# Performance work log

Measured on AMD Instinct MI355X. Metric: run time of the kernel, lower is better.

Reference implementation:

```python
import jax, jax.numpy as jnp
import numpy as np
import math

E = 2048        # embed_dim
H = 16          # num_heads
HD = E // H // 2  # head_dim = 64
DEPTH = 12
LAMBDA_INIT = 0.8 - 0.6 * math.exp(-0.3 * DEPTH)


def setup_inputs() -> dict:
    key = jax.random.key(0)
    ks = jax.random.split(key, 9)
    s = 0.02
    return {
        "x": jax.random.normal(ks[0], (2, 2048, E), jnp.float32),
        "Wq": jax.random.normal(ks[1], (E, E), jnp.float32) * s,
        "Wk": jax.random.normal(ks[2], (E, E), jnp.float32) * s,  # n_rep = 1
        "Wv": jax.random.normal(ks[3], (E, E), jnp.float32) * s,
        "Wo": jax.random.normal(ks[4], (E, E), jnp.float32) * s,
        "lq1": jax.random.normal(ks[5], (HD,), jnp.float32) * 0.1,
        "lk1": jax.random.normal(ks[6], (HD,), jnp.float32) * 0.1,
        "lq2": jax.random.normal(ks[7], (HD,), jnp.float32) * 0.1,
        "lk2": jax.random.normal(ks[8], (HD,), jnp.float32) * 0.1,
    }


def reference(x, Wq, Wk, Wv, Wo, lq1, lk1, lq2, lk2):
    b, t, e = x.shape
    scaling = HD ** (-0.5)
    # projections; split into 2*H sub-heads of dim HD for q/k, H heads of 2*HD for v
    q = (x @ Wq).reshape(b, t, 2 * H, HD).transpose(0, 2, 1, 3) * scaling  # [b,2H,t,hd]
    k = (x @ Wk).reshape(b, t, 2 * H, HD).transpose(0, 2, 1, 3)           # [b,2H,t,hd]
    v = (x @ Wv).reshape(b, t, H, 2 * HD).transpose(0, 2, 1, 3)           # [b,H,t,2hd]

    scores = jnp.einsum('bhqd,bhkd->bhqk', q, k)  # [b,2H,t,t]
    causal = jnp.triu(jnp.full((t, t), -jnp.inf, dtype=jnp.float32), 1)
    aw = jax.nn.softmax((scores + causal).astype(jnp.float32), axis=-1)

    lam = (jnp.exp(jnp.sum(lq1 * lk1)) - jnp.exp(jnp.sum(lq2 * lk2)) + LAMBDA_INIT)
    aw = aw.reshape(b, H, 2, t, t)
    aw = aw[:, :, 0] - lam * aw[:, :, 1]  # differential attention

    attn = jnp.einsum('bhqk,bhkd->bhqd', aw, v)  # [b,H,t,2hd]
    # RMSNorm over last dim (no affine), eps=1e-5
    attn = attn * jax.lax.rsqrt(jnp.mean(attn * attn, axis=-1, keepdims=True) + 1e-5)
    attn = attn * (1.0 - LAMBDA_INIT)
    attn = attn.transpose(0, 2, 1, 3).reshape(b, t, H * 2 * HD)
    return attn @ Wo
```

## Files before the change

kernel.cpp:

```cpp
#include <hip/hip_runtime.h>
#include <stdint.h>

typedef __bf16 bf16_t;
typedef __bf16 bf16x8 __attribute__((ext_vector_type(8)));
typedef __bf16 bf16x4 __attribute__((ext_vector_type(4)));
typedef float  f32x4  __attribute__((ext_vector_type(4)));

#define L2E 1.44269504088896340736f
#define LAMBDA_INIT 0.7836057665316245f
#define ONE_MINUS_LAMBDA_INIT 0.2163942334683755f

__device__ __forceinline__ void gload_lds16(const void* g, void* l) {
  __builtin_amdgcn_global_load_lds(
      (const __attribute__((address_space(1))) char*)(uintptr_t)g,
      (__attribute__((address_space(3))) char*)(uintptr_t)l, 16, 0, 0);
}

__device__ __forceinline__ f32x4 mfma_bf16(bf16x8 a, bf16x8 b, f32x4 c) {
  return __builtin_amdgcn_mfma_f32_16x16x32_bf16(a, b, c, 0, 0, 0);
}

__global__ __launch_bounds__(256) void cvt_bf16(const float* __restrict__ in,
                                                bf16_t* __restrict__ out) {
  const size_t idx = ((size_t)blockIdx.x * 256 + threadIdx.x) * 8;
  float4 a = *(const float4*)(in + idx);
  float4 c = *(const float4*)(in + idx + 4);
  bf16x8 v;
  v[0] = (bf16_t)a.x; v[1] = (bf16_t)a.y; v[2] = (bf16_t)a.z; v[3] = (bf16_t)a.w;
  v[4] = (bf16_t)c.x; v[5] = (bf16_t)c.y; v[6] = (bf16_t)c.z; v[7] = (bf16_t)c.w;
  *(bf16x8*)(out + idx) = v;
}

__global__ __launch_bounds__(256) void cvt_wT(const float* __restrict__ W,
                                              bf16_t* __restrict__ WT, float scale) {
  __shared__ float t[64][65];
  const int k0 = blockIdx.x * 64, n0 = blockIdx.y * 64;
  const int r = threadIdx.x >> 2, cg = threadIdx.x & 3;
#pragma unroll
  for (int q = 0; q < 4; ++q) {
    float4 v = *(const float4*)(W + (size_t)(k0 + r) * 2048 + n0 + cg * 16 + q * 4);
    t[r][cg * 16 + q * 4 + 0] = v.x;
    t[r][cg * 16 + q * 4 + 1] = v.y;
    t[r][cg * 16 + q * 4 + 2] = v.z;
    t[r][cg * 16 + q * 4 + 3] = v.w;
  }
  __syncthreads();
  bf16x8 o0, o1;
#pragma unroll
  for (int j = 0; j < 8; ++j) o0[j] = (bf16_t)(t[cg * 16 + j][r] * scale);
#pragma unroll
  for (int j = 0; j < 8; ++j) o1[j] = (bf16_t)(t[cg * 16 + 8 + j][r] * scale);
  bf16_t* dst = WT + (size_t)(n0 + r) * 2048 + k0 + cg * 16;
  *(bf16x8*)dst = o0;
  *(bf16x8*)(dst + 8) = o1;
}

__global__ void lam_kernel(const float* lq1, const float* lk1,
                           const float* lq2, const float* lk2, float* out) {
  const int l = threadIdx.x;
  float p1 = lq1[l] * lk1[l];
  float p2 = lq2[l] * lk2[l];
#pragma unroll
  for (int d = 1; d < 64; d <<= 1) {
    p1 += __shfl_xor(p1, d);
    p2 += __shfl_xor(p2, d);
  }
  if (l == 0) *out = expf(p1) - expf(p2) + LAMBDA_INIT;
}

template <int OUTMODE>
__global__ __launch_bounds__(256, 2) void gemm_bt(const bf16_t* __restrict__ A,
                                                  const bf16_t* __restrict__ Bt,
                                                  void* __restrict__ Cv) {
  __shared__ __align__(16) bf16_t As[128 * 64];
  __shared__ __align__(16) bf16_t Bs[128 * 64];
  const int tid = threadIdx.x;
  const int w = tid >> 6, lane = tid & 63;
  const int wr = w >> 1, wc = w & 1;
  const int lm = lane >> 4, ln = lane & 15;
  const int flat = (int)blockIdx.y * (int)gridDim.x + (int)blockIdx.x;
  const int swz = (flat & 7) * 64 + (flat >> 3);
  const int m0 = (swz & 31) * 128, n0 = (swz >> 5) * 128;

  const f32x4 vzero = {0.f, 0.f, 0.f, 0.f};
  f32x4 acc[4][4];
#pragma unroll
  for (int m = 0; m < 4; ++m)
#pragma unroll
    for (int n = 0; n < 4; ++n) acc[m][n] = vzero;

  for (int k0 = 0; k0 < 2048; k0 += 64) {
    __syncthreads();
#pragma unroll
    for (int j = 0; j < 4; ++j) {
      const int inst = w * 4 + j;
      const int row = inst * 8 + (lane >> 3);
      const int cb = ((lane & 7) * 16) ^ ((row & 7) << 4);
      gload_lds16(A + (size_t)(m0 + row) * 2048 + k0 + (cb >> 1),
                  (char*)As + inst * 1024);
      gload_lds16(Bt + (size_t)(n0 + row) * 2048 + k0 + (cb >> 1),
                  (char*)Bs + inst * 1024);
    }
    asm volatile("s_waitcnt vmcnt(0)" ::: "memory");
    __syncthreads();

#pragma unroll
    for (int kc = 0; kc < 2; ++kc) {
      bf16x8 af[4], bfr[4];
#pragma unroll
      for (int m = 0; m < 4; ++m) {
        const int row = wr * 64 + m * 16 + ln;
        int off = row * 128 + kc * 64 + lm * 16;
        off ^= (row & 7) << 4;
        af[m] = *(const bf16x8*)((const char*)As + off);
      }
#pragma unroll
      for (int n = 0; n < 4; ++n) {
        const int row = wc * 64 + n * 16 + ln;
        int off = row * 128 + kc * 64 + lm * 16;
        off ^= (row & 7) << 4;
        bfr[n] = *(const bf16x8*)((const char*)Bs + off);
      }
      __builtin_amdgcn_s_setprio(1);
#pragma unroll
      for (int m = 0; m < 4; ++m)
#pragma unroll
        for (int n = 0; n < 4; ++n) acc[m][n] = mfma_bf16(af[m], bfr[n], acc[m][n]);
      __builtin_amdgcn_s_setprio(0);
    }
  }

  if (OUTMODE == 0) {
    bf16_t* C = (bf16_t*)Cv;
#pragma unroll
    for (int m = 0; m < 4; ++m)
#pragma unroll
      for (int n = 0; n < 4; ++n)
#pragma unroll
        for (int r = 0; r < 4; ++r) {
          const size_t grow = m0 + wr * 64 + m * 16 + lm * 4 + r;
          const int gcol = n0 + wc * 64 + n * 16 + ln;
          C[grow * 2048 + gcol] = (bf16_t)acc[m][n][r];
        }
  } else if (OUTMODE == 1) {
    bf16_t* C = (bf16_t*)Cv;
#pragma unroll
    for (int m = 0; m < 4; ++m)
#pragma unroll
      for (int n = 0; n < 4; ++n) {
        const size_t gcol = n0 + wc * 64 + n * 16 + ln;
        const int growb = m0 + wr * 64 + m * 16 + lm * 4;
        bf16x4 v;
#pragma unroll
        for (int r = 0; r < 4; ++r) v[r] = (bf16_t)acc[m][n][r];
        *(bf16x4*)(C + gcol * 4096 + growb) = v;
      }
  } else {
    float* C = (float*)Cv;
#pragma unroll
    for (int m = 0; m < 4; ++m)
#pragma unroll
      for (int n = 0; n < 4; ++n)
#pragma unroll
        for (int r = 0; r < 4; ++r) {
          const size_t grow = m0 + wr * 64 + m * 16 + lm * 4 + r;
          const int gcol = n0 + wc * 64 + n * 16 + ln;
          C[grow * 2048 + gcol] = acc[m][n][r];
        }
  }
}

__global__ __launch_bounds__(256, 2) void flash_diff(const bf16_t* __restrict__ Q,
                                                     const bf16_t* __restrict__ K,
                                                     const bf16_t* __restrict__ Vt,
                                                     bf16_t* __restrict__ attnb,
                                                     const float* __restrict__ lamP) {
  __shared__ __align__(16) char smem[81920];
  bf16_t* Ps = (bf16_t*)smem;

  const int tid = threadIdx.x;
  const int w = tid >> 6, lane = tid & 63;
  const int lm = lane >> 4, ln = lane & 15;
  const int h = blockIdx.y, b = blockIdx.z;
  const size_t bt0 = (size_t)b * 2048;
  const float lam = *lamP;

  auto stage_kv = [&](int buf, int k0) {
#pragma unroll
    for (int j = 0; j < 4; ++j) {
      const int inst = w * 4 + j;
      {
        const int row = inst * 4 + (lane >> 4);
        const int cb = ((lane & 15) * 16) ^ ((row & 7) << 4);
        gload_lds16(K + (bt0 + k0 + row) * 2048 + h * 128 + (cb >> 1),
                    smem + 16384 + buf * 16384 + inst * 1024);
      }
      {
        const int row = inst * 8 + (lane >> 3);
        const int cb = ((lane & 7) * 16) ^ ((row & 7) << 4);
        gload_lds16(Vt + (size_t)(h * 128 + row) * 4096 + bt0 + k0 + (cb >> 1),
                    smem + 49152 + buf * 16384 + inst * 1024);
      }
    }
  };

  for (int half = 0; half < 2; ++half) {
    const int qt = half == 0 ? (int)blockIdx.x : 31 - (int)blockIdx.x;
    const int q0 = qt * 64;

#pragma unroll
    for (int j = 0; j < 4; ++j) {
      const int inst = w * 4 + j;
      const int row = inst * 4 + (lane >> 4);
      const int cb = ((lane & 15) * 16) ^ ((row & 7) << 4);
      gload_lds16(Q + (bt0 + q0 + row) * 2048 + h * 128 + (cb >> 1),
                  smem + inst * 1024);
    }
    stage_kv(0, 0);
    asm volatile("s_waitcnt vmcnt(0)" ::: "memory");
    __syncthreads();

    bf16x8 qf[2][2];
#pragma unroll
    for (int s = 0; s < 2; ++s)
#pragma unroll
      for (int kc = 0; kc < 2; ++kc) {
        const int row = w * 16 + ln;
        int off = row * 256 + s * 128 + kc * 64 + lm * 16;
        off ^= (row & 7) << 4;
        qf[s][kc] = *(const bf16x8*)((const char*)smem + off);
      }
    __syncthreads();

    const f32x4 vzero = {0.f, 0.f, 0.f, 0.f};
    f32x4 acc[2][8];
    float lsum[2][4];
#pragma unroll
    for (int s = 0; s < 2; ++s) {
#pragma unroll
      for (int n = 0; n < 8; ++n) acc[s][n] = vzero;
#pragma unroll
      for (int r = 0; r < 4; ++r) lsum[s][r] = 0.f;
    }

    int cur = 0;
    for (int kt = 0; kt <= qt; ++kt) {
      if (kt < qt) stage_kv(cur ^ 1, (kt + 1) * 64);

      const char* Ksb = (const char*)smem + 16384 + cur * 16384;
      const char* Vsb = (const char*)smem + 49152 + cur * 16384;

#pragma unroll
      for (int s = 0; s < 2; ++s) {
        f32x4 sa[4];
#pragma unroll
        for (int n = 0; n < 4; ++n) sa[n] = vzero;
        __builtin_amdgcn_s_setprio(1);
#pragma unroll
        for (int kc = 0; kc < 2; ++kc) {
#pragma unroll
          for (int n = 0; n < 4; ++n) {
            const int row = n * 16 + ln;
            int off = row * 256 + s * 128 + kc * 64 + lm * 16;
            off ^= (row & 7) << 4;
            bf16x8 kf = *(const bf16x8*)(Ksb + off);
            sa[n] = mfma_bf16(qf[s][kc], kf, sa[n]);
          }
        }
        __builtin_amdgcn_s_setprio(0);
        if (kt == qt) {
#pragma unroll
          for (int n = 0; n < 4; ++n)
#pragma unroll
            for (int r = 0; r < 4; ++r) {
              const int kg = n * 16 + ln;
              const int qg = w * 16 + lm * 4 + r;
              if (kg > qg) sa[n][r] = -1e30f;
            }
        }
        bf16_t* pbase = Ps + (w * 2 + s) * 1024;
#pragma unroll
        for (int r = 0; r < 4; ++r) {
          float ps = 0.f;
#pragma unroll
          for (int n = 0; n < 4; ++n) {
            const float p = exp2f(sa[n][r]);
            sa[n][r] = p;
            ps += p;
          }
          lsum[s][r] += ps;
        }
#pragma unroll
        for (int n = 0; n < 4; ++n)
#pragma unroll
          for (int r = 0; r < 4; ++r) {
            const int row = lm * 4 + r;
            int off = row * 128 + (n * 16 + ln) * 2;
            off ^= (row & 7) << 4;
            *(bf16_t*)((char*)pbase + off) = (bf16_t)sa[n][r];
          }
      }

#pragma unroll
      for (int kc = 0; kc < 2; ++kc) {
        bf16x8 pf[2];
#pragma unroll
        for (int s = 0; s < 2; ++s) {
          int off = ln * 128 + kc * 64 + lm * 16;
          off ^= (ln & 7) << 4;
          pf[s] = *(const bf16x8*)((const char*)(Ps + (w * 2 + s) * 1024) + off);
        }
        __builtin_amdgcn_s_setprio(1);
#pragma unroll
        for (int n = 0; n < 8; ++n) {
          const int row = n * 16 + ln;
          int off = row * 128 + kc * 64 + lm * 16;
          off ^= (row & 7) << 4;
          bf16x8 vf = *(const bf16x8*)(Vsb + off);
          acc[0][n] = mfma_bf16(pf[0], vf, acc[0][n]);
          acc[1][n] = mfma_bf16(pf[1], vf, acc[1][n]);
        }
        __builtin_amdgcn_s_setprio(0);
      }

      asm volatile("s_waitcnt vmcnt(0)" ::: "memory");
      __syncthreads();
      cur ^= 1;
    }

#pragma unroll
    for (int r = 0; r < 4; ++r) {
      float l0 = lsum[0][r], l1 = lsum[1][r];
#pragma unroll
      for (int d = 1; d < 16; d <<= 1) {
        l0 += __shfl_xor(l0, d);
        l1 += __shfl_xor(l1, d);
      }
      const float rl0 = 1.0f / l0;
      const float rl1 = 1.0f / l1;
      float o[8];
      float ss = 0.f;
#pragma unroll
      for (int n = 0; n < 8; ++n) {
        const float v = acc[0][n][r] * rl0 - lam * (acc[1][n][r] * rl1);
        o[n] = v;
        ss += v * v;
      }
      ss += __shfl_xor(ss, 1);
      ss += __shfl_xor(ss, 2);
      ss += __shfl_xor(ss, 4);
      ss += __shfl_xor(ss, 8);
      const float sc = rsqrtf(ss * (1.0f / 128.f) + 1e-5f) * ONE_MINUS_LAMBDA_INIT;
      const size_t grow = bt0 + q0 + w * 16 + lm * 4 + r;
#pragma unroll
      for (int n = 0; n < 8; ++n)
        attnb[grow * 2048 + h * 128 + n * 16 + ln] = (bf16_t)(o[n] * sc);
    }
  }
}

extern "C" void kernel_launch(void* const* d_in, const int* in_sizes, int n_in,
                              void* d_out, int out_size, void* d_ws, size_t ws_size,
                              hipStream_t stream) {
  const float* x   = (const float*)d_in[0];
  const float* Wq  = (const float*)d_in[1];
  const float* Wk  = (const float*)d_in[2];
  const float* Wv  = (const float*)d_in[3];
  const float* Wo  = (const float*)d_in[4];
  const float* lq1 = (const float*)d_in[5];
  const float* lk1 = (const float*)d_in[6];
  const float* lq2 = (const float*)d_in[7];
  const float* lk2 = (const float*)d_in[8];

  char* ws = (char*)d_ws;
  bf16_t* xb    = (bf16_t*)(ws + 0);
  bf16_t* wqT   = (bf16_t*)(ws + 16777216);
  bf16_t* wkT   = (bf16_t*)(ws + 25165824);
  bf16_t* wvT   = (bf16_t*)(ws + 33554432);
  bf16_t* woT   = (bf16_t*)(ws + 41943040);
  bf16_t* Qb    = (bf16_t*)(ws + 50331648);
  bf16_t* Kb    = (bf16_t*)(ws + 67108864);
  bf16_t* Vtb   = (bf16_t*)(ws + 16777216);
  bf16_t* attnb = (bf16_t*)(ws + 0);
  float*  lamP  = (float*)(ws + 83886080);

  cvt_bf16<<<4096, 256, 0, stream>>>(x, xb);
  cvt_wT<<<dim3(32, 32), 256, 0, stream>>>(Wq, wqT, 0.125f * L2E);
  cvt_wT<<<dim3(32, 32), 256, 0, stream>>>(Wk, wkT, 1.0f);
  cvt_wT<<<dim3(32, 32), 256, 0, stream>>>(Wv, wvT, 1.0f);
  cvt_wT<<<dim3(32, 32), 256, 0, stream>>>(Wo, woT, 1.0f);
  lam_kernel<<<1, 64, 0, stream>>>(lq1, lk1, lq2, lk2, lamP);

  gemm_bt<0><<<dim3(32, 16), 256, 0, stream>>>(xb, wqT, (void*)Qb);
  gemm_bt<0><<<dim3(32, 16), 256, 0, stream>>>(xb, wkT, (void*)Kb);
  gemm_bt<1><<<dim3(32, 16), 256, 0, stream>>>(xb, wvT, (void*)Vtb);

  flash_diff<<<dim3(16, 16, 2), 256, 0, stream>>>(Qb, Kb, Vtb, attnb, lamP);

  gemm_bt<2><<<dim3(32, 16), 256, 0, stream>>>(attnb, woT, d_out);
}
```

Before: 287.9 us.

## Rewrite flash_diff with 32x32 MFMA, register-resident P via permlane swap

Restructures the differential flash attention kernel so each wave handles 32 queries for one sub-head using 32x32x16 MFMA. It computes S transposed (K·Q), so the exponentiated probabilities are packed to bf16 and rearranged with v_permlane32_swap into the B operand of the PV MFMA, with no LDS round trip for P. The two sub-head outputs are combined at the end through an LDS buffer, which adds extra syncs. This removes the P store/load LDS traffic and per-row shuffles, but raises register pressure from the 64-float accumulators.

Measured after the change: 288.5 us. No clear change (+0.2%).

```diff
diff --git a/kernel.cpp b/kernel.cpp
--- a/kernel.cpp
+++ b/kernel.cpp
@@ -5,6 +5,8 @@
 typedef __bf16 bf16x8 __attribute__((ext_vector_type(8)));
 typedef __bf16 bf16x4 __attribute__((ext_vector_type(4)));
 typedef float  f32x4  __attribute__((ext_vector_type(4)));
+typedef float  f32x16 __attribute__((ext_vector_type(16)));
+typedef unsigned int u32;
 
 #define L2E 1.44269504088896340736f
 #define LAMBDA_INIT 0.7836057665316245f
@@ -18,6 +20,18 @@
 
 __device__ __forceinline__ f32x4 mfma_bf16(bf16x8 a, bf16x8 b, f32x4 c) {
   return __builtin_amdgcn_mfma_f32_16x16x32_bf16(a, b, c, 0, 0, 0);
+}
+__device__ __forceinline__ f32x16 mfma32(bf16x8 a, bf16x8 b, f32x16 c) {
+  return __builtin_amdgcn_mfma_f32_32x32x16_bf16(a, b, c, 0, 0, 0);
+}
+
+__device__ __forceinline__ u32 pkbf(float a, float b) {
+  union { bf16_t h[2]; u32 u; } x;
+  x.h[0] = (bf16_t)a; x.h[1] = (bf16_t)b;
+  return x.u;
+}
+__device__ __forceinline__ void pl32swap(u32& a, u32& b) {
+  asm volatile("v_permlane32_swap_b32 %0, %1" : "+v"(a), "+v"(b));
 }
 
 __global__ __launch_bounds__(256) void cvt_bf16(const float* __restrict__ in,
@@ -176,11 +190,11 @@
                                                      bf16_t* __restrict__ attnb,
                                                      const float* __restrict__ lamP) {
   __shared__ __align__(16) char smem[81920];
-  bf16_t* Ps = (bf16_t*)smem;
 
   const int tid = threadIdx.x;
   const int w = tid >> 6, lane = tid & 63;
-  const int lm = lane >> 4, ln = lane & 15;
+  const int qh = w >> 1, s = w & 1;
+  const int l31 = lane & 31, hi = lane >> 5;
   const int h = blockIdx.y, b = blockIdx.z;
   const size_t bt0 = (size_t)b * 2048;
   const float lam = *lamP;
@@ -207,6 +221,7 @@
   for (int half = 0; half < 2; ++half) {
     const int qt = half == 0 ? (int)blockIdx.x : 31 - (int)blockIdx.x;
     const int q0 = qt * 64;
+    const int qloc = qh * 32 + l31;
 
 #pragma unroll
     for (int j = 0; j < 4; ++j) {
@@ -220,28 +235,21 @@
     asm volatile("s_waitcnt vmcnt(0)" ::: "memory");
     __syncthreads();
 
-    bf16x8 qf[2][2];
-#pragma unroll
-    for (int s = 0; s < 2; ++s)
-#pragma unroll
-      for (int kc = 0; kc < 2; ++kc) {
-        const int row = w * 16 + ln;
-        int off = row * 256 + s * 128 + kc * 64 + lm * 16;
-        off ^= (row & 7) << 4;
-        qf[s][kc] = *(const bf16x8*)((const char*)smem + off);
-      }
-    __syncthreads();
-
-    const f32x4 vzero = {0.f, 0.f, 0.f, 0.f};
-    f32x4 acc[2][8];
-    float lsum[2][4];
-#pragma unroll
-    for (int s = 0; s < 2; ++s) {
-#pragma unroll
-      for (int n = 0; n < 8; ++n) acc[s][n] = vzero;
-#pragma unroll
-      for (int r = 0; r < 4; ++r) lsum[s][r] = 0.f;
-    }
+    bf16x8 qf[4];
+#pragma unroll
+    for (int kc = 0; kc < 4; ++kc) {
+      const int row = qloc;
+      int off = row * 256 + s * 128 + kc * 32 + hi * 16;
+      off ^= (row & 7) << 4;
+      qf[kc] = *(const bf16x8*)((const char*)smem + off);
+    }
+
+    f32x16 accv[4];
+#pragma unroll
+    for (int m = 0; m < 4; ++m)
+#pragma unroll
+      for (int r = 0; r < 16; ++r) accv[m][r] = 0.f;
+    float lsum = 0.f;
 
     int cur = 0;
     for (int kt = 0; kt <= qt; ++kt) {
@@ -250,112 +258,125 @@
       const char* Ksb = (const char*)smem + 16384 + cur * 16384;
       const char* Vsb = (const char*)smem + 49152 + cur * 16384;
 
-#pragma unroll
-      for (int s = 0; s < 2; ++s) {
-        f32x4 sa[4];
-#pragma unroll
-        for (int n = 0; n < 4; ++n) sa[n] = vzero;
-        __builtin_amdgcn_s_setprio(1);
-#pragma unroll
-        for (int kc = 0; kc < 2; ++kc) {
-#pragma unroll
-          for (int n = 0; n < 4; ++n) {
-            const int row = n * 16 + ln;
-            int off = row * 256 + s * 128 + kc * 64 + lm * 16;
-            off ^= (row & 7) << 4;
-            bf16x8 kf = *(const bf16x8*)(Ksb + off);
-            sa[n] = mfma_bf16(qf[s][kc], kf, sa[n]);
+      f32x16 sa[2];
+#pragma unroll
+      for (int m = 0; m < 2; ++m)
+#pragma unroll
+        for (int r = 0; r < 16; ++r) sa[m][r] = 0.f;
+      __builtin_amdgcn_s_setprio(1);
+#pragma unroll
+      for (int kc = 0; kc < 4; ++kc) {
+#pragma unroll
+        for (int mt = 0; mt < 2; ++mt) {
+          const int row = mt * 32 + l31;
+          int off = row * 256 + s * 128 + kc * 32 + hi * 16;
+          off ^= (row & 7) << 4;
+          bf16x8 kf = *(const bf16x8*)(Ksb + off);
+          sa[mt] = mfma32(kf, qf[kc], sa[mt]);
+        }
+      }
+      __builtin_amdgcn_s_setprio(0);
+
+      if (kt == qt) {
+#pragma unroll
+        for (int mt = 0; mt < 2; ++mt)
+#pragma unroll
+          for (int r = 0; r < 16; ++r) {
+            const int key = mt * 32 + (r & 3) + 8 * (r >> 2) + 4 * hi;
+            if (key > qloc) sa[mt][r] = -1e30f;
           }
-        }
-        __builtin_amdgcn_s_setprio(0);
-        if (kt == qt) {
-#pragma unroll
-          for (int n = 0; n < 4; ++n)
-#pragma unroll
-            for (int r = 0; r < 4; ++r) {
-              const int kg = n * 16 + ln;
-              const int qg = w * 16 + lm * 4 + r;
-              if (kg > qg) sa[n][r] = -1e30f;
-            }
-        }
-        bf16_t* pbase = Ps + (w * 2 + s) * 1024;
-#pragma unroll
-        for (int r = 0; r < 4; ++r) {
-          float ps = 0.f;
-#pragma unroll
-          for (int n = 0; n < 4; ++n) {
-            const float p = exp2f(sa[n][r]);
-            sa[n][r] = p;
-            ps += p;
-          }
-          lsum[s][r] += ps;
-        }
-#pragma unroll
-        for (int n = 0; n < 4; ++n)
-#pragma unroll
-          for (int r = 0; r < 4; ++r) {
-            const int row = lm * 4 + r;
-            int off = row * 128 + (n * 16 + ln) * 2;
-            off ^= (row & 7) << 4;
-            *(bf16_t*)((char*)pbase + off) = (bf16_t)sa[n][r];
-          }
-      }
-
-#pragma unroll
-      for (int kc = 0; kc < 2; ++kc) {
-        bf16x8 pf[2];
-#pragma unroll
-        for (int s = 0; s < 2; ++s) {
-          int off = ln * 128 + kc * 64 + lm * 16;
-          off ^= (ln & 7) << 4;
-          pf[s] = *(const bf16x8*)((const char*)(Ps + (w * 2 + s) * 1024) + off);
-        }
-        __builtin_amdgcn_s_setprio(1);
-#pragma unroll
-        for (int n = 0; n < 8; ++n) {
-          const int row = n * 16 + ln;
-          int off = row * 128 + kc * 64 + lm * 16;
-          off ^= (row & 7) << 4;
+      }
+
+      bf16x8 pf[2][2];
+#pragma unroll
+      for (int mt = 0; mt < 2; ++mt) {
+        float p[16];
+#pragma unroll
+        for (int r = 0; r < 16; ++r) {
+          p[r] = exp2f(sa[mt][r]);
+          lsum += p[r];
+        }
+        u32 c0 = pkbf(p[0], p[1]),   c1 = pkbf(p[2], p[3]);
+        u32 c2 = pkbf(p[4], p[5]),   c3 = pkbf(p[6], p[7]);
+        u32 c4 = pkbf(p[8], p[9]),   c5 = pkbf(p[10], p[11]);
+        u32 c6 = pkbf(p[12], p[13]), c7 = pkbf(p[14], p[15]);
+        pl32swap(c0, c2); pl32swap(c1, c3);
+        pl32swap(c4, c6); pl32swap(c5, c7);
+        union { u32 u[4]; bf16x8 v; } f0, f1;
+        f0.u[0] = c0; f0.u[1] = c1; f0.u[2] = c2; f0.u[3] = c3;
+        f1.u[0] = c4; f1.u[1] = c5; f1.u[2] = c6; f1.u[3] = c7;
+        pf[mt][0] = f0.v;
+        pf[mt][1] = f1.v;
+      }
+
+      __builtin_amdgcn_s_setprio(1);
+#pragma unroll
+      for (int mt4 = 0; mt4 < 4; ++mt4) {
+        const int row = mt4 * 32 + l31;
+        const int rswz = (row & 7) << 4;
+#pragma unroll
+        for (int st = 0; st < 4; ++st) {
+          int off = row * 128 + st * 32 + hi * 16;
+          off ^= rswz;
           bf16x8 vf = *(const bf16x8*)(Vsb + off);
-          acc[0][n] = mfma_bf16(pf[0], vf, acc[0][n]);
-          acc[1][n] = mfma_bf16(pf[1], vf, acc[1][n]);
-        }
-        __builtin_amdgcn_s_setprio(0);
-      }
+          accv[mt4] = mfma32(vf, pf[st >> 1][st & 1], accv[mt4]);
+        }
+      }
+      __builtin_amdgcn_s_setprio(0);
 
       asm volatile("s_waitcnt vmcnt(0)" ::: "memory");
       __syncthreads();
       cur ^= 1;
     }
 
-#pragma unroll
-    for (int r = 0; r < 4; ++r) {
-      float l0 = lsum[0][r], l1 = lsum[1][r];
-#pragma unroll
-      for (int d = 1; d < 16; d <<= 1) {
-        l0 += __shfl_xor(l0, d);
-        l1 += __shfl_xor(l1, d);
-      }
-      const float rl0 = 1.0f / l0;
-      const float rl1 = 1.0f / l1;
-      float o[8];
+    lsum += __shfl_xor(lsum, 32);
+    const float rl = 1.0f / lsum;
+    float* Obuf = (float*)(smem + 16384);
+
+    if (s == 1) {
+#pragma unroll
+      for (int mt4 = 0; mt4 < 4; ++mt4)
+#pragma unroll
+        for (int q2 = 0; q2 < 4; ++q2) {
+          f32x4 v;
+#pragma unroll
+          for (int e = 0; e < 4; ++e) v[e] = accv[mt4][q2 * 4 + e] * rl;
+          const int d = mt4 * 32 + q2 * 8 + hi * 4;
+          *(f32x4*)(Obuf + (size_t)qloc * 128 + d) = v;
+        }
+    }
+    __syncthreads();
+    if (s == 0) {
+      float o[4][16];
       float ss = 0.f;
 #pragma unroll
-      for (int n = 0; n < 8; ++n) {
-        const float v = acc[0][n][r] * rl0 - lam * (acc[1][n][r] * rl1);
-        o[n] = v;
-        ss += v * v;
-      }
-      ss += __shfl_xor(ss, 1);
-      ss += __shfl_xor(ss, 2);
-      ss += __shfl_xor(ss, 4);
-      ss += __shfl_xor(ss, 8);
+      for (int mt4 = 0; mt4 < 4; ++mt4)
+#pragma unroll
+        for (int q2 = 0; q2 < 4; ++q2) {
+          const int d = mt4 * 32 + q2 * 8 + hi * 4;
+          f32x4 ov = *(const f32x4*)(Obuf + (size_t)qloc * 128 + d);
+#pragma unroll
+          for (int e = 0; e < 4; ++e) {
+            const float v = accv[mt4][q2 * 4 + e] * rl - lam * ov[e];
+            o[mt4][q2 * 4 + e] = v;
+            ss += v * v;
+          }
+        }
+      ss += __shfl_xor(ss, 32);
       const float sc = rsqrtf(ss * (1.0f / 128.f) + 1e-5f) * ONE_MINUS_LAMBDA_INIT;
-      const size_t grow = bt0 + q0 + w * 16 + lm * 4 + r;
-#pragma unroll
-      for (int n = 0; n < 8; ++n)
-        attnb[grow * 2048 + h * 128 + n * 16 + ln] = (bf16_t)(o[n] * sc);
-    }
+      const size_t grow = bt0 + q0 + qloc;
+#pragma unroll
+      for (int mt4 = 0; mt4 < 4; ++mt4)
+#pragma unroll
+        for (int q2 = 0; q2 < 4; ++q2) {
+          const int d = mt4 * 32 + q2 * 8 + hi * 4;
+          bf16x4 v;
+#pragma unroll
+          for (int e = 0; e < 4; ++e) v[e] = (bf16_t)(o[mt4][q2 * 4 + e] * sc);
+          *(bf16x4*)(attnb + grow * 2048 + h * 128 + d) = v;
+        }
+    }
+    __syncthreads();
   }
 }
 
```
